# Kernel tuning notes

Hardware: AMD Instinct MI355X
Metric: run time of the kernel (lower is better)

The kernel has to match this reference:

```python
import jax, jax.numpy as jnp
import numpy as np

N = 250_000   # nodes per graph batch
E = 4_000_000 # edges
G = 1024      # graphs (segments)
F_IN, C, D = 6, 64, 5
EPS = 1e-5    # PyG LayerNorm eps


def setup_inputs() -> dict:
    key = jax.random.key(0)
    ks = jax.random.split(key, 30)
    rn = lambda k, s: jax.random.normal(k, s, jnp.float32)
    p = lambda k, s: rn(k, s) * 0.05
    return {
        "x1": rn(ks[0], (N, F_IN)),
        "edge_index1": jax.random.randint(ks[1], (2, E), 0, N, jnp.int32),
        "batch1": jnp.sort(jax.random.randint(ks[2], (N,), 0, G, jnp.int32)),
        "x2": rn(ks[3], (N, F_IN)),
        "edge_index2": jax.random.randint(ks[4], (2, E), 0, N, jnp.int32),
        "batch2": jnp.sort(jax.random.randint(ks[5], (N,), 0, G, jnp.int32)),
        "d1": rn(ks[6], (G, D)),
        "d2": rn(ks[7], (G, D)),
        # GIN MLP 1: Linear(6,64) -> ReLU -> Linear(64,64)
        "W1": p(ks[8], (F_IN, C)), "b1": jnp.zeros((C,), jnp.float32),
        "W2": p(ks[9], (C, C)),    "b2": jnp.zeros((C,), jnp.float32),
        "ln1w": jnp.ones((C,), jnp.float32), "ln1b": jnp.zeros((C,), jnp.float32),
        # GIN MLP 2
        "W3": p(ks[10], (C, C)), "b3": jnp.zeros((C,), jnp.float32),
        "W4": p(ks[11], (C, C)), "b4": jnp.zeros((C,), jnp.float32),
        "ln2w": jnp.ones((C,), jnp.float32), "ln2b": jnp.zeros((C,), jnp.float32),
        # head: Linear(138,128) -> Linear(128,64) -> Linear(64,1)
        "Wf1": p(ks[12], (2 * C + 2 * D, 128)), "bf1": jnp.zeros((128,), jnp.float32),
        "Wf2": p(ks[13], (128, 64)),            "bf2": jnp.zeros((64,), jnp.float32),
        "Wo": p(ks[14], (64, 1)),               "bo": jnp.zeros((1,), jnp.float32),
    }


def _gin(x, src, dst, Wa, ba, Wb, bb):
    # GINConv, eps=0: h = x + sum_{j in N(i)} x_j ; then MLP (dropout = eval identity)
    agg = jax.ops.segment_sum(x[src], dst, num_segments=N)
    h = x + agg
    h = jax.nn.relu(h @ Wa + ba)
    return h @ Wb + bb


def _graph_layernorm(x, batch, w, b):
    # PyG LayerNorm mode='graph': normalize over all nodes AND channels per graph
    cnt = jax.ops.segment_sum(jnp.ones((x.shape[0],), x.dtype), batch, num_segments=G)
    norm = jnp.maximum(cnt, 1.0) * x.shape[-1]          # [G]
    mean = jax.ops.segment_sum(x.sum(-1), batch, num_segments=G) / norm
    xc = x - mean[batch][:, None]
    var = jax.ops.segment_sum((xc * xc).sum(-1), batch, num_segments=G) / norm
    out = xc * jax.lax.rsqrt(var + EPS)[batch][:, None]
    return out * w + b


def _forward_one(x, edge_index, batch, W1, b1, W2, b2, ln1w, ln1b, W3, b3, W4, b4, ln2w, ln2b):
    src, dst = edge_index[0], edge_index[1]
    x = jax.nn.relu(_graph_layernorm(_gin(x, src, dst, W1, b1, W2, b2), batch, ln1w, ln1b))
    x = jax.nn.relu(_graph_layernorm(_gin(x, src, dst, W3, b3, W4, b4), batch, ln2w, ln2b))
    add = jax.ops.segment_sum(x, batch, num_segments=G)  # [G, C]
    cnt = jax.ops.segment_sum(jnp.ones((x.shape[0],), x.dtype), batch, num_segments=G)
    mean = add / jnp.maximum(cnt, 1.0)[:, None]
    return add + mean


def reference(x1, edge_index1, batch1, x2, edge_index2, batch2, d1, d2,
              W1, b1, W2, b2, ln1w, ln1b, W3, b3, W4, b4, ln2w, ln2b,
              Wf1, bf1, Wf2, bf2, Wo, bo):
    shared = (W1, b1, W2, b2, ln1w, ln1b, W3, b3, W4, b4, ln2w, ln2b)
    emb1 = _forward_one(x1, edge_index1, batch1, *shared)
    emb2 = _forward_one(x2, edge_index2, batch2, *shared)
    h = jnp.concatenate([emb1, emb2, d1, d2], axis=1)    # [G, 138]
    h = jax.nn.relu(h @ Wf1 + bf1)                       # dropout identity (eval)
    h = jax.nn.relu(h @ Wf2 + bf2)
    return h @ Wo + bo                                   # [G, 1]
```

## Files before the change

kernel.cpp:

```cpp
#include <hip/hip_runtime.h>

typedef unsigned short ushort_t;
typedef __attribute__((ext_vector_type(8))) short bf16x8;
typedef __attribute__((ext_vector_type(4))) float f32x4;

#define FIN 6
#define CAP 20480
#define LNCAP 384

__device__ __forceinline__ float blo(unsigned u) { return __uint_as_float(u << 16); }
__device__ __forceinline__ float bhi(unsigned u) { return __uint_as_float(u & 0xffff0000u); }
__device__ __forceinline__ ushort_t f2b(float f) {
  unsigned u = __float_as_uint(f);
  unsigned r = (u + 0x7fffu + ((u >> 16) & 1u)) >> 16;
  return (ushort_t)r;
}
__device__ __forceinline__ unsigned pk2(float lo, float hi) {
  return ((unsigned)f2b(hi) << 16) | (unsigned)f2b(lo);
}
union U4F { uint4 u; bf16x8 v; };
__device__ __forceinline__ bf16x8 asfrag(uint4 u) { U4F x; x.u = u; return x.v; }

__device__ __forceinline__ int xcd_swz(int b, int B) {
  int xcd = b & 7, sub = b >> 3;
  int bpx = B >> 3;
  return (xcd >> 2) * (B >> 1) + (xcd & 3) * bpx + sub;
}

#define EPT 16
#define TILE 8192

__global__ __launch_bounds__(256) void k_wpack(const float* __restrict__ W2,
    const float* __restrict__ W3, const float* __restrict__ W4, uint4* __restrict__ wfrag,
    int* __restrict__ ecur, int* __restrict__ off, int nbuk, int N2, int Etot,
    const float* __restrict__ x1, const float* __restrict__ x2,
    const int* __restrict__ batch1, const int* __restrict__ batch2,
    unsigned* __restrict__ xb, int* __restrict__ gstart, int N, int G) {
  if (blockIdx.x >= 7) {
    int G2 = 2 * G;
    int tt = (blockIdx.x - 7) * 256 + threadIdx.x;
    if (tt < N2 * 4) {
      int i = tt >> 2, k = tt & 3;
      unsigned v = 0;
      if (k < 3) {
        const float* xp = (i < N) ? (x1 + (size_t)i * 6) : (x2 + (size_t)(i - N) * 6);
        float2 f = *(const float2*)(xp + k * 2);
        v = pk2(f.x, f.y);
      }
      xb[tt] = v;
    }
    if (tt < N2) {
      int i = tt;
      int b = (i < N) ? batch1[i] : (batch2[i - N] + G);
      if (i == 0) { for (int g = 0; g <= b; ++g) gstart[g] = 0; }
      else {
        int pb = (i - 1 < N) ? batch1[i - 1] : (batch2[i - 1 - N] + G);
        for (int g = pb + 1; g <= b; ++g) gstart[g] = i;
      }
      if (i == N2 - 1) { for (int g = b + 1; g <= G2; ++g) gstart[g] = N2; }
    }
    return;
  }
  if (blockIdx.x == 6) {
    int t = threadIdx.x;
    if (t < nbuk) ecur[t] = t * CAP;
    if (t + 256 < nbuk) ecur[t + 256] = (t + 256) * CAP;
    if (t == 0) off[N2] = Etot;
    return;
  }
  int idx = blockIdx.x * 256 + threadIdx.x;
  if (idx >= 3 * 512) return;
  int widx = idx >> 9, rem = idx & 511;
  int mt = rem >> 7, kh = (rem >> 6) & 1, l = rem & 63;
  int g = l >> 4, c = l & 15;
  const float* W = (widx == 0) ? W2 : (widx == 1) ? W3 : W4;
  int k0 = kh * 32 + g * 8;
  int col = mt * 16 + c;
  uint4 v;
  v.x = pk2(W[(k0 + 0) * 64 + col], W[(k0 + 1) * 64 + col]);
  v.y = pk2(W[(k0 + 2) * 64 + col], W[(k0 + 3) * 64 + col]);
  v.z = pk2(W[(k0 + 4) * 64 + col], W[(k0 + 5) * 64 + col]);
  v.w = pk2(W[(k0 + 6) * 64 + col], W[(k0 + 7) * 64 + col]);
  wfrag[idx] = v;
}

__global__ __launch_bounds__(512) void k_bscatter(
    const int* __restrict__ src1, const int* __restrict__ dst1, int E1,
    const int* __restrict__ src2, const int* __restrict__ dst2, int E2,
    int* __restrict__ ecur, unsigned* __restrict__ ebuf, int N, int nbuk) {
  __shared__ int cnt[512];
  __shared__ int gbase[512];
  int t = threadIdx.x;
  cnt[t] = 0;
  __syncthreads();
  int tile = blockIdx.x;
  int T1 = (E1 + TILE - 1) / TILE;
  const int* srcp; const int* dstp; int Elim, ofs, base;
  if (tile < T1) { srcp = src1; dstp = dst1; Elim = E1; ofs = 0; base = tile * TILE; }
  else { srcp = src2; dstp = dst2; Elim = E2; ofs = N; base = (tile - T1) * TILE; }
  unsigned pk[EPT];
  unsigned pv[EPT];
  #pragma unroll
  for (int k = 0; k < EPT; ++k) {
    int e = base + k * 512 + t;
    if (e < Elim) {
      int d = dstp[e] + ofs;
      int b = d >> 10;
      int r = atomicAdd(&cnt[b], 1);
      pk[k] = (unsigned)b | ((unsigned)r << 9);
      pv[k] = ((unsigned)(d & 1023) << 19) | (unsigned)(srcp[e] + ofs);
    } else {
      pk[k] = 0xFFFFFFFFu;
    }
  }
  __syncthreads();
  if (t < nbuk && cnt[t] > 0) gbase[t] = atomicAdd(&ecur[t], cnt[t]);
  __syncthreads();
  #pragma unroll
  for (int k = 0; k < EPT; ++k) {
    if (pk[k] != 0xFFFFFFFFu) {
      int b = pk[k] & 511;
      int r = pk[k] >> 9;
      ebuf[gbase[b] + r] = pv[k];
    }
  }
}

__global__ __launch_bounds__(512) void k_bscan2(const int* __restrict__ ecur,
    int* __restrict__ ebase, int nbuk) {
  __shared__ int lds[512];
  int t = threadIdx.x;
  int s = (t < nbuk) ? (ecur[t] - t * CAP) : 0;
  lds[t] = s; __syncthreads();
  int acc = s;
  for (int o = 1; o < 512; o <<= 1) {
    int add = (t >= o) ? lds[t - o] : 0;
    __syncthreads();
    acc += add; lds[t] = acc;
    __syncthreads();
  }
  if (t < nbuk) ebase[t] = acc - s;
}

__global__ __launch_bounds__(256) void k_bcsr(const unsigned* __restrict__ ebuf,
    const int* __restrict__ ecur, const int* __restrict__ ebase,
    int* __restrict__ off, int* __restrict__ csr, int N2) {
  __shared__ int hist[1024];
  __shared__ int lofs[1024];
  __shared__ int sc[256];
  int b = blockIdx.x, t = threadIdx.x;
  int nb0 = b << 10;
  int bn = N2 - nb0; if (bn > 1024) bn = 1024;
  int s_beg = b * CAP, s_end = ecur[b];
  int base = ebase[b];
  #pragma unroll
  for (int k = 0; k < 4; ++k) hist[t * 4 + k] = 0;
  __syncthreads();
  for (int e = s_beg + t; e < s_end; e += 256) atomicAdd(&hist[ebuf[e] >> 19], 1);
  __syncthreads();
  int h0 = hist[t * 4 + 0], h1 = hist[t * 4 + 1], h2 = hist[t * 4 + 2], h3 = hist[t * 4 + 3];
  int s = h0 + h1 + h2 + h3;
  sc[t] = s; __syncthreads();
  int acc = s;
  for (int o = 1; o < 256; o <<= 1) {
    int add = (t >= o) ? sc[t - o] : 0;
    __syncthreads();
    acc += add; sc[t] = acc;
    __syncthreads();
  }
  int run = acc - s;
  lofs[t * 4 + 0] = run; run += h0;
  lofs[t * 4 + 1] = run; run += h1;
  lofs[t * 4 + 2] = run; run += h2;
  lofs[t * 4 + 3] = run;
  __syncthreads();
  #pragma unroll
  for (int k = 0; k < 4; ++k) {
    int j = t * 4 + k;
    if (j < bn) off[nb0 + j] = base + lofs[j];
  }
  __syncthreads();
  for (int e = s_beg + t; e < s_end; e += 256) {
    unsigned p = ebuf[e];
    int r = atomicAdd(&lofs[p >> 19], 1);
    csr[base + r] = (int)(p & 0x7FFFFu);
  }
}

#define ACC6(u) { a0 += blo(u.x); a1 += bhi(u.x); a2 += blo(u.y); a3 += bhi(u.y); a4 += blo(u.z); a5 += bhi(u.z); }
__global__ __launch_bounds__(256) void k_gin1f(const uint4* __restrict__ xb4,
    const int* __restrict__ off, const int* __restrict__ csr,
    const float* __restrict__ W1, const float* __restrict__ b1,
    const uint4* __restrict__ wf2, const float* __restrict__ b2,
    ushort_t* __restrict__ hr, int n) {
  __shared__ __align__(16) ushort_t t1s[32][72];
  __shared__ float sh[4][8][FIN];
  int t = threadIdx.x, w = t >> 6, lane = t & 63;
  int nd = lane >> 3, sl = lane & 7;
  int blk = xcd_swz(blockIdx.x, gridDim.x);
  int nb0 = blk * 32;
  int i = nb0 + w * 8 + nd;

  float w1r[FIN];
  #pragma unroll
  for (int k = 0; k < FIN; ++k) w1r[k] = W1[k * 64 + lane];
  float bb1 = b1[lane];

  float a0 = 0, a1 = 0, a2 = 0, a3 = 0, a4 = 0, a5 = 0;
  if (i < n) {
    int e0 = off[i], e1 = off[i + 1];
    int e = e0 + sl;
    for (; e + 8 < e1; e += 16) {
      uint4 u = xb4[csr[e]];
      uint4 v = xb4[csr[e + 8]];
      ACC6(u); ACC6(v);
    }
    if (e < e1) { uint4 u = xb4[csr[e]]; ACC6(u); }
    if (sl == 0) { uint4 u = xb4[i]; ACC6(u); }
  }
  #pragma unroll
  for (int m = 1; m < 8; m <<= 1) {
    a0 += __shfl_xor(a0, m); a1 += __shfl_xor(a1, m); a2 += __shfl_xor(a2, m);
    a3 += __shfl_xor(a3, m); a4 += __shfl_xor(a4, m); a5 += __shfl_xor(a5, m);
  }
  if (sl < FIN) {
    float v = (sl == 0) ? a0 : (sl == 1) ? a1 : (sl == 2) ? a2 : (sl == 3) ? a3 : (sl == 4) ? a4 : a5;
    sh[w][nd][sl] = v;
  }
  #pragma unroll
  for (int nd2 = 0; nd2 < 8; ++nd2) {
    float h = bb1;
    #pragma unroll
    for (int k = 0; k < FIN; ++k) h = fmaf(sh[w][nd2][k], w1r[k], h);
    t1s[w * 8 + nd2][lane] = f2b(fmaxf(h, 0.f));
  }
  __syncthreads();
  if (w < 2) {
    int g = lane >> 4, c = lane & 15;
    bf16x8 af[4][2];
    #pragma unroll
    for (int mt = 0; mt < 4; ++mt)
      #pragma unroll
      for (int kh = 0; kh < 2; ++kh) af[mt][kh] = asfrag(wf2[(mt * 2 + kh) * 64 + lane]);
    int r0 = w * 16 + c;
    bf16x8 bf0 = asfrag(*(const uint4*)&t1s[r0][8 * g]);
    bf16x8 bf1 = asfrag(*(const uint4*)&t1s[r0][8 * g + 32]);
    f32x4 acc[4];
    #pragma unroll
    for (int mt = 0; mt < 4; ++mt) {
      acc[mt] = (f32x4){b2[mt * 16 + 4 * g + 0], b2[mt * 16 + 4 * g + 1],
                        b2[mt * 16 + 4 * g + 2], b2[mt * 16 + 4 * g + 3]};
      acc[mt] = __builtin_amdgcn_mfma_f32_16x16x32_bf16(af[mt][0], bf0, acc[mt], 0, 0, 0);
      acc[mt] = __builtin_amdgcn_mfma_f32_16x16x32_bf16(af[mt][1], bf1, acc[mt], 0, 0, 0);
    }
    #pragma unroll
    for (int mt = 0; mt < 4; ++mt) {
      uint2 pv;
      pv.x = pk2(acc[mt][0], acc[mt][1]);
      pv.y = pk2(acc[mt][2], acc[mt][3]);
      *(uint2*)&t1s[r0][mt * 16 + 4 * g] = pv;
    }
    int n2 = lane >> 2, ch = (lane & 3) * 16;
    uint4 s0 = *(const uint4*)&t1s[w * 16 + n2][ch];
    uint4 s1 = *(const uint4*)&t1s[w * 16 + n2][ch + 8];
    int orow = nb0 + w * 16 + n2;
    if (orow < n) {
      uint4* op = (uint4*)(hr + (size_t)orow * 64);
      op[(lane & 3) * 2] = s0;
      op[(lane & 3) * 2 + 1] = s1;
    }
  }
}

__device__ __forceinline__ float2 up2(unsigned v) { return make_float2(blo(v), bhi(v)); }
#define PACC(u) { float2 q0 = up2(u.x), q1 = up2(u.y), q2 = up2(u.z), q3 = up2(u.w); \
                  c0.x += q0.x; c0.y += q0.y; c1.x += q1.x; c1.y += q1.y; \
                  c2.x += q2.x; c2.y += q2.y; c3.x += q3.x; c3.y += q3.y; }
__global__ __launch_bounds__(256) void k_agg64(const ushort_t* __restrict__ hb,
    const int* __restrict__ off, const int* __restrict__ csr,
    ushort_t* __restrict__ aggb, int n) {
  int t = threadIdx.x, w = t >> 6, lane = t & 63;
  int blk = xcd_swz(blockIdx.x, gridDim.x);
  int i = blk * 4 + w;
  if (i >= n) return;
  int grp = lane >> 3, sl = lane & 7;
  int e0 = off[i], e1 = off[i + 1];
  const uint4* hb4 = (const uint4*)hb;
  float2 c0 = {0, 0}, c1 = {0, 0}, c2 = {0, 0}, c3 = {0, 0};
  int e = e0 + grp;
  for (; e + 8 < e1; e += 16) {
    int sa = csr[e], sb = csr[e + 8];
    uint4 ua = hb4[(size_t)sa * 8 + sl];
    uint4 ub = hb4[(size_t)sb * 8 + sl];
    PACC(ua); PACC(ub);
  }
  if (e < e1) {
    int sa = csr[e];
    uint4 ua = hb4[(size_t)sa * 8 + sl];
    PACC(ua);
  }
  #pragma unroll
  for (int m = 8; m < 64; m <<= 1) {
    c0.x += __shfl_xor(c0.x, m); c0.y += __shfl_xor(c0.y, m);
    c1.x += __shfl_xor(c1.x, m); c1.y += __shfl_xor(c1.y, m);
    c2.x += __shfl_xor(c2.x, m); c2.y += __shfl_xor(c2.y, m);
    c3.x += __shfl_xor(c3.x, m); c3.y += __shfl_xor(c3.y, m);
  }
  if (grp == 0) {
    uint4 us = hb4[(size_t)i * 8 + sl];
    PACC(us);
    uint4 o;
    o.x = pk2(c0.x, c0.y); o.y = pk2(c1.x, c1.y);
    o.z = pk2(c2.x, c2.y); o.w = pk2(c3.x, c3.y);
    ((uint4*)aggb)[(size_t)i * 8 + sl] = o;
  }
}

__global__ __launch_bounds__(256) void k_mlp2_mfma(const ushort_t* __restrict__ aggb,
    const uint4* __restrict__ wf3, const float* __restrict__ b3,
    const uint4* __restrict__ wf4, const float* __restrict__ b4,
    ushort_t* __restrict__ zb, int n) {
  __shared__ __align__(16) ushort_t lds[4][16][72];
  int t = threadIdx.x, w = t >> 6, l = t & 63;
  int g = l >> 4, c = l & 15;
  bf16x8 a3[4][2], a4[4][2];
  #pragma unroll
  for (int mt = 0; mt < 4; ++mt)
    #pragma unroll
    for (int kh = 0; kh < 2; ++kh) {
      a3[mt][kh] = asfrag(wf3[(mt * 2 + kh) * 64 + l]);
      a4[mt][kh] = asfrag(wf4[(mt * 2 + kh) * 64 + l]);
    }
  float bs3[4][4], bs4[4][4];
  #pragma unroll
  for (int mt = 0; mt < 4; ++mt)
    #pragma unroll
    for (int r = 0; r < 4; ++r) {
      bs3[mt][r] = b3[mt * 16 + 4 * g + r];
      bs4[mt][r] = b4[mt * 16 + 4 * g + r];
    }
  int ntile = (n + 15) >> 4;
  for (int tau = blockIdx.x * 4 + w; tau < ntile; tau += gridDim.x * 4) {
    int nb = tau << 4;
    int row = nb + c; if (row >= n) row = n - 1;
    const uint4* rp = (const uint4*)(aggb + (size_t)row * 64);
    bf16x8 bf0 = asfrag(rp[g]);
    bf16x8 bf1 = asfrag(rp[g + 4]);
    f32x4 acc[4];
    #pragma unroll
    for (int mt = 0; mt < 4; ++mt) {
      acc[mt] = (f32x4){bs3[mt][0], bs3[mt][1], bs3[mt][2], bs3[mt][3]};
      acc[mt] = __builtin_amdgcn_mfma_f32_16x16x32_bf16(a3[mt][0], bf0, acc[mt], 0, 0, 0);
      acc[mt] = __builtin_amdgcn_mfma_f32_16x16x32_bf16(a3[mt][1], bf1, acc[mt], 0, 0, 0);
    }
    #pragma unroll
    for (int mt = 0; mt < 4; ++mt) {
      uint2 pv;
      pv.x = pk2(fmaxf(acc[mt][0], 0.f), fmaxf(acc[mt][1], 0.f));
      pv.y = pk2(fmaxf(acc[mt][2], 0.f), fmaxf(acc[mt][3], 0.f));
      *(uint2*)&lds[w][c][mt * 16 + 4 * g] = pv;
    }
    bf16x8 h0 = asfrag(*(const uint4*)&lds[w][c][8 * g]);
    bf16x8 h1 = asfrag(*(const uint4*)&lds[w][c][8 * g + 32]);
    f32x4 ac2[4];
    #pragma unroll
    for (int mt = 0; mt < 4; ++mt) {
      ac2[mt] = (f32x4){bs4[mt][0], bs4[mt][1], bs4[mt][2], bs4[mt][3]};
      ac2[mt] = __builtin_amdgcn_mfma_f32_16x16x32_bf16(a4[mt][0], h0, ac2[mt], 0, 0, 0);
      ac2[mt] = __builtin_amdgcn_mfma_f32_16x16x32_bf16(a4[mt][1], h1, ac2[mt], 0, 0, 0);
    }
    #pragma unroll
    for (int mt = 0; mt < 4; ++mt) {
      uint2 pv;
      pv.x = pk2(ac2[mt][0], ac2[mt][1]);
      pv.y = pk2(ac2[mt][2], ac2[mt][3]);
      *(uint2*)&lds[w][c][mt * 16 + 4 * g] = pv;
    }
    int n2 = l >> 2, ch = (l & 3) * 16;
    uint4 s0 = *(const uint4*)&lds[w][n2][ch];
    uint4 s1 = *(const uint4*)&lds[w][n2][ch + 8];
    int orow = nb + n2;
    if (orow < n) {
      uint4* op = (uint4*)(zb + (size_t)orow * 64);
      op[(l & 3) * 2] = s0;
      op[(l & 3) * 2 + 1] = s1;
    }
  }
}

__global__ __launch_bounds__(256) void k_ln1(ushort_t* __restrict__ hr,
    const int* __restrict__ gstart, const float* __restrict__ w, const float* __restrict__ bb) {
  __shared__ uint4 st[LNCAP * 8];
  __shared__ float l1[256], l2[256];
  __shared__ float mm[2];
  int g = blockIdx.x, t = threadIdx.x;
  int s0 = gstart[g], s1 = gstart[g + 1], cnt = s1 - s0;
  uint4* src = (uint4*)hr + (size_t)s0 * 8;
  int nch = cnt * 8;
  bool fit = cnt <= LNCAP;
  float s = 0.f, ss = 0.f;
  for (int j = t; j < nch; j += 256) {
    uint4 u = src[j];
    if (fit) st[j] = u;
    float v0 = blo(u.x), v1 = bhi(u.x), v2 = blo(u.y), v3 = bhi(u.y);
    float v4 = blo(u.z), v5 = bhi(u.z), v6 = blo(u.w), v7 = bhi(u.w);
    s += ((v0 + v1) + (v2 + v3)) + ((v4 + v5) + (v6 + v7));
    ss += ((v0 * v0 + v1 * v1) + (v2 * v2 + v3 * v3)) + ((v4 * v4 + v5 * v5) + (v6 * v6 + v7 * v7));
  }
  l1[t] = s; l2[t] = ss;
  __syncthreads();
  for (int o = 128; o > 0; o >>= 1) {
    if (t < o) { l1[t] += l1[t + o]; l2[t] += l2[t + o]; }
    __syncthreads();
  }
  if (t == 0) {
    float cf = (float)cnt;
    float norm = fmaxf(cf, 1.f) * 64.f;
    float mean = l1[0] / norm;
    float var = fmaxf(l2[0] / norm - mean * mean, 0.f);
    mm[0] = mean; mm[1] = rsqrtf(var + 1e-5f);
  }
  __syncthreads();
  float mean = mm[0], inv = mm[1];
  for (int j = t; j < nch; j += 256) {
    uint4 u = fit ? st[j] : src[j];
    int q = j & 7;
    float4 w0 = *(const float4*)(w + q * 8);
    float4 w1 = *(const float4*)(w + q * 8 + 4);
    float4 c0 = *(const float4*)(bb + q * 8);
    float4 c1 = *(const float4*)(bb + q * 8 + 4);
    uint4 o;
    o.x = pk2(fmaxf((blo(u.x) - mean) * inv * w0.x + c0.x, 0.f),
              fmaxf((bhi(u.x) - mean) * inv * w0.y + c0.y, 0.f));
    o.y = pk2(fmaxf((blo(u.y) - mean) * inv * w0.z + c0.z, 0.f),
              fmaxf((bhi(u.y) - mean) * inv * w0.w + c0.w, 0.f));
    o.z = pk2(fmaxf((blo(u.z) - mean) * inv * w1.x + c1.x, 0.f),
              fmaxf((bhi(u.z) - mean) * inv * w1.y + c1.y, 0.f));
    o.w = pk2(fmaxf((blo(u.w) - mean) * inv * w1.z + c1.z, 0.f),
              fmaxf((bhi(u.w) - mean) * inv * w1.w + c1.w, 0.f));
    src[j] = o;
  }
}

__global__ __launch_bounds__(256) void k_ln2pool(const ushort_t* __restrict__ zb,
    const int* __restrict__ gstart, const float* __restrict__ w, const float* __restrict__ bb,
    float* __restrict__ emb) {
  __shared__ unsigned st[LNCAP * 32];
  __shared__ float l1[256], l2[256];
  __shared__ float mm[2];
  int g = blockIdx.x, t = threadIdx.x;
  int s0 = gstart[g], s1 = gstart[g + 1], cnt = s1 - s0;
  const unsigned* src = (const unsigned*)zb + (size_t)s0 * 32;
  int nu = cnt * 32;
  bool fit = cnt <= LNCAP;
  float s = 0.f, ss = 0.f;
  for (int j = t; j < nu; j += 256) {
    unsigned u = src[j];
    if (fit) st[j] = u;
    float v0 = blo(u), v1 = bhi(u);
    s += v0 + v1;
    ss += v0 * v0 + v1 * v1;
  }
  l1[t] = s; l2[t] = ss;
  __syncthreads();
  for (int o = 128; o > 0; o >>= 1) {
    if (t < o) { l1[t] += l1[t + o]; l2[t] += l2[t + o]; }
    __syncthreads();
  }
  if (t == 0) {
    float cf = (float)cnt;
    float norm = fmaxf(cf, 1.f) * 64.f;
    float mean = l1[0] / norm;
    float var = fmaxf(l2[0] / norm - mean * mean, 0.f);
    mm[0] = mean; mm[1] = rsqrtf(var + 1e-5f);
  }
  __syncthreads();
  float mean = mm[0], inv = mm[1];
  int c2 = t & 31, sub = t >> 5;
  float w0 = w[c2 * 2], w1 = w[c2 * 2 + 1], b0 = bb[c2 * 2], b1v = bb[c2 * 2 + 1];
  float acc0 = 0.f, acc1 = 0.f;
  for (int i = sub; i < cnt; i += 8) {
    unsigned u = fit ? st[i * 32 + c2] : src[(size_t)i * 32 + c2];
    acc0 += fmaxf((blo(u) - mean) * inv * w0 + b0, 0.f);
    acc1 += fmaxf((bhi(u) - mean) * inv * w1 + b1v, 0.f);
  }
  __syncthreads();
  l1[t] = acc0; l2[t] = acc1;
  __syncthreads();
  if (sub == 0) {
    float t0 = 0.f, t1v = 0.f;
    #pragma unroll
    for (int sx = 0; sx < 8; ++sx) { t0 += l1[sx * 32 + c2]; t1v += l2[sx * 32 + c2]; }
    float cf = fmaxf((float)cnt, 1.f);
    emb[g * 64 + c2 * 2]     = t0 + t0 / cf;
    emb[g * 64 + c2 * 2 + 1] = t1v + t1v / cf;
  }
}

__global__ __launch_bounds__(128) void k_head(const float* __restrict__ emb1,
    const float* __restrict__ emb2, const float* __restrict__ d1, const float* __restrict__ d2,
    const float* __restrict__ Wf1, const float* __restrict__ bf1,
    const float* __restrict__ Wf2, const float* __restrict__ bf2,
    const float* __restrict__ Wo, const float* __restrict__ bo, float* __restrict__ out) {
  int g = blockIdx.x, t = threadIdx.x;
  __shared__ float v[138], h1s[128], h2s[64];
  if (t < 64) v[t] = emb1[g * 64 + t];
  else v[t] = emb2[g * 64 + (t - 64)];
  if (t < 5) v[128 + t] = d1[g * 5 + t];
  else if (t < 10) v[133 + (t - 5)] = d2[g * 5 + (t - 5)];
  __syncthreads();
  float a = bf1[t];
  for (int k = 0; k < 138; ++k) a = fmaf(v[k], Wf1[k * 128 + t], a);
  h1s[t] = fmaxf(a, 0.f);
  __syncthreads();
  if (t < 64) {
    float a2 = bf2[t];
    #pragma unroll 8
    for (int k = 0; k < 128; ++k) a2 = fmaf(h1s[k], Wf2[k * 64 + t], a2);
    h2s[t] = fmaxf(a2, 0.f);
  }
  __syncthreads();
  if (t == 0) {
    float s = bo[0];
    for (int k = 0; k < 64; ++k) s += h2s[k] * Wo[k];
    out[g] = s;
  }
}

extern "C" void kernel_launch(void* const* d_in, const int* in_sizes, int n_in,
                              void* d_out, int out_size, void* d_ws, size_t ws_size,
                              hipStream_t stream) {
  const float* x1     = (const float*)d_in[0];
  const int*   ei1    = (const int*)d_in[1];
  const int*   batch1 = (const int*)d_in[2];
  const float* x2     = (const float*)d_in[3];
  const int*   ei2    = (const int*)d_in[4];
  const int*   batch2 = (const int*)d_in[5];
  const float* d1     = (const float*)d_in[6];
  const float* d2     = (const float*)d_in[7];
  const float* W1  = (const float*)d_in[8],  *b1  = (const float*)d_in[9];
  const float* W2  = (const float*)d_in[10], *b2  = (const float*)d_in[11];
  const float* ln1w = (const float*)d_in[12], *ln1b = (const float*)d_in[13];
  const float* W3  = (const float*)d_in[14], *b3  = (const float*)d_in[15];
  const float* W4  = (const float*)d_in[16], *b4  = (const float*)d_in[17];
  const float* ln2w = (const float*)d_in[18], *ln2b = (const float*)d_in[19];
  const float* Wf1 = (const float*)d_in[20], *bf1 = (const float*)d_in[21];
  const float* Wf2 = (const float*)d_in[22], *bf2 = (const float*)d_in[23];
  const float* Wo  = (const float*)d_in[24], *bo  = (const float*)d_in[25];
  float* out = (float*)d_out;

  const int N = in_sizes[0] / FIN;
  const int G = in_sizes[6] / 5;
  const int E1 = in_sizes[1] / 2;
  const int E2 = in_sizes[4] / 2;
  const int N2 = 2 * N;
  const int Etot = E1 + E2;
  const int NBUK = (N2 + 1023) >> 10;

  char* p = (char*)d_ws;
  auto alloc = [&](size_t bytes) { void* r = p; p += (bytes + 255) & ~(size_t)255; return r; };
  int*      off    = (int*)alloc((size_t)(N2 + 1) * 4);
  int*      ecur   = (int*)alloc(512 * 4);
  int*      ebase  = (int*)alloc(513 * 4);
  int*      csr    = (int*)alloc((size_t)Etot * 4);
  int*      gstart = (int*)alloc((size_t)(2 * G + 1) * 4);
  uint4*    wfrag  = (uint4*)alloc(3 * 512 * 16);
  ushort_t* bufA   = (ushort_t*)alloc((size_t)N2 * 64 * 2);
  ushort_t* bufB   = (ushort_t*)alloc((size_t)N2 * 64 * 2);
  float*    emb    = (float*)alloc((size_t)2 * G * 64 * 4);

  unsigned* xb   = (unsigned*)bufB;
  unsigned* ebuf = (unsigned*)((char*)bufB + (size_t)N2 * 16);
  ushort_t* hr   = bufA;
  ushort_t* aggb = bufB;
  ushort_t* zb   = bufA;

  const uint4* wf2 = wfrag;
  const uint4* wf3 = wfrag + 512;
  const uint4* wf4 = wfrag + 1024;

  const int SCAT   = (E1 + TILE - 1) / TILE + (E2 + TILE - 1) / TILE;
  const int GRID_F = (((N2 + 31) / 32) + 7) & ~7;
  const int GRID_W = (((N2 + 3) / 4) + 7) & ~7;
  const int GRID_P = (N2 * 4 + 255) / 256;

  k_wpack<<<7 + GRID_P, 256, 0, stream>>>(W2, W3, W4, wfrag, ecur, off, NBUK, N2, Etot,
                                          x1, x2, batch1, batch2, xb, gstart, N, G);
  k_bscatter<<<SCAT, 512, 0, stream>>>(ei1, ei1 + E1, E1, ei2, ei2 + E2, E2, ecur, ebuf, N, NBUK);
  k_bscan2<<<1, 512, 0, stream>>>(ecur, ebase, NBUK);
  k_bcsr<<<NBUK, 256, 0, stream>>>(ebuf, ecur, ebase, off, csr, N2);

  k_gin1f<<<GRID_F, 256, 0, stream>>>((const uint4*)xb, off, csr, W1, b1, wf2, b2, hr, N2);
  k_ln1<<<2 * G, 256, 0, stream>>>(hr, gstart, ln1w, ln1b);
  k_agg64<<<GRID_W, 256, 0, stream>>>(hr, off, csr, aggb, N2);
  k_mlp2_mfma<<<2048, 256, 0, stream>>>(aggb, wf3, b3, wf4, b4, zb, N2);
  k_ln2pool<<<2 * G, 256, 0, stream>>>(zb, gstart, ln2w, ln2b, emb);

  k_head<<<G, 128, 0, stream>>>(emb, emb + (size_t)G * 64, d1, d2, Wf1, bf1, Wf2, bf2, Wo, bo, out);
}
```

Measured before the change: 547.7 us.

## Split destination buckets into source-range sub-buckets to sort CSR by source

```diff
diff --git a/kernel.cpp b/kernel.cpp
--- a/kernel.cpp
+++ b/kernel.cpp
@@ -5,7 +5,8 @@
 typedef __attribute__((ext_vector_type(4))) float f32x4;
 
 #define FIN 6
-#define CAP 20480
+#define CAPS 1408
+#define NSUBMAX 8192
 #define LNCAP 384
 
 __device__ __forceinline__ float blo(unsigned u) { return __uint_as_float(u << 16); }
@@ -32,7 +33,7 @@
 
 __global__ __launch_bounds__(256) void k_wpack(const float* __restrict__ W2,
     const float* __restrict__ W3, const float* __restrict__ W4, uint4* __restrict__ wfrag,
-    int* __restrict__ ecur, int* __restrict__ off, int nbuk, int N2, int Etot,
+    int* __restrict__ ecur, int* __restrict__ off, int N2, int Etot,
     const float* __restrict__ x1, const float* __restrict__ x2,
     const int* __restrict__ batch1, const int* __restrict__ batch2,
     unsigned* __restrict__ xb, int* __restrict__ gstart, int N, int G) {
@@ -62,10 +63,8 @@
     return;
   }
   if (blockIdx.x == 6) {
-    int t = threadIdx.x;
-    if (t < nbuk) ecur[t] = t * CAP;
-    if (t + 256 < nbuk) ecur[t + 256] = (t + 256) * CAP;
-    if (t == 0) off[N2] = Etot;
+    for (int j = threadIdx.x; j < NSUBMAX; j += 256) ecur[j] = j * CAPS;
+    if (threadIdx.x == 0) off[N2] = Etot;
     return;
   }
   int idx = blockIdx.x * 256 + threadIdx.x;
@@ -87,11 +86,10 @@
 __global__ __launch_bounds__(512) void k_bscatter(
     const int* __restrict__ src1, const int* __restrict__ dst1, int E1,
     const int* __restrict__ src2, const int* __restrict__ dst2, int E2,
-    int* __restrict__ ecur, unsigned* __restrict__ ebuf, int N, int nbuk) {
-  __shared__ int cnt[512];
-  __shared__ int gbase[512];
+    int* __restrict__ ecur, unsigned* __restrict__ ebuf, int N, int nsub) {
+  __shared__ int cnt[NSUBMAX];
   int t = threadIdx.x;
-  cnt[t] = 0;
+  for (int j = t; j < NSUBMAX; j += 512) cnt[j] = 0;
   __syncthreads();
   int tile = blockIdx.x;
   int T1 = (E1 + TILE - 1) / TILE;
@@ -104,24 +102,28 @@
   for (int k = 0; k < EPT; ++k) {
     int e = base + k * 512 + t;
     if (e < Elim) {
+      int sl = srcp[e];
       int d = dstp[e] + ofs;
-      int b = d >> 10;
-      int r = atomicAdd(&cnt[b], 1);
-      pk[k] = (unsigned)b | ((unsigned)r << 9);
-      pv[k] = ((unsigned)(d & 1023) << 19) | (unsigned)(srcp[e] + ofs);
+      int sub = ((d >> 10) << 4) | (sl >> 14);
+      int r = atomicAdd(&cnt[sub], 1);
+      pk[k] = (unsigned)sub | ((unsigned)r << 13);
+      pv[k] = ((unsigned)(d & 1023) << 19) | (unsigned)(sl + ofs);
     } else {
       pk[k] = 0xFFFFFFFFu;
     }
   }
   __syncthreads();
-  if (t < nbuk && cnt[t] > 0) gbase[t] = atomicAdd(&ecur[t], cnt[t]);
+  for (int j = t; j < nsub; j += 512) {
+    int c = cnt[j];
+    if (c > 0) cnt[j] = atomicAdd(&ecur[j], c);
+  }
   __syncthreads();
   #pragma unroll
   for (int k = 0; k < EPT; ++k) {
     if (pk[k] != 0xFFFFFFFFu) {
-      int b = pk[k] & 511;
-      int r = pk[k] >> 9;
-      ebuf[gbase[b] + r] = pv[k];
+      int sub = pk[k] & (NSUBMAX - 1);
+      int r = pk[k] >> 13;
+      ebuf[cnt[sub] + r] = pv[k];
     }
   }
 }
@@ -130,7 +132,14 @@
     int* __restrict__ ebase, int nbuk) {
   __shared__ int lds[512];
   int t = threadIdx.x;
-  int s = (t < nbuk) ? (ecur[t] - t * CAP) : 0;
+  int s = 0;
+  if (t < nbuk) {
+    #pragma unroll
+    for (int sl = 0; sl < 16; ++sl) {
+      int sub = t * 16 + sl;
+      s += ecur[sub] - sub * CAPS;
+    }
+  }
   lds[t] = s; __syncthreads();
   int acc = s;
   for (int o = 1; o < 512; o <<= 1) {
@@ -151,12 +160,15 @@
   int b = blockIdx.x, t = threadIdx.x;
   int nb0 = b << 10;
   int bn = N2 - nb0; if (bn > 1024) bn = 1024;
-  int s_beg = b * CAP, s_end = ecur[b];
   int base = ebase[b];
   #pragma unroll
   for (int k = 0; k < 4; ++k) hist[t * 4 + k] = 0;
   __syncthreads();
-  for (int e = s_beg + t; e < s_end; e += 256) atomicAdd(&hist[ebuf[e] >> 19], 1);
+  for (int sl = 0; sl < 16; ++sl) {
+    int sub = (b << 4) | sl;
+    int s_beg = sub * CAPS, s_end = ecur[sub];
+    for (int e = s_beg + t; e < s_end; e += 256) atomicAdd(&hist[ebuf[e] >> 19], 1);
+  }
   __syncthreads();
   int h0 = hist[t * 4 + 0], h1 = hist[t * 4 + 1], h2 = hist[t * 4 + 2], h3 = hist[t * 4 + 3];
   int s = h0 + h1 + h2 + h3;
@@ -180,10 +192,15 @@
     if (j < bn) off[nb0 + j] = base + lofs[j];
   }
   __syncthreads();
-  for (int e = s_beg + t; e < s_end; e += 256) {
-    unsigned p = ebuf[e];
-    int r = atomicAdd(&lofs[p >> 19], 1);
-    csr[base + r] = (int)(p & 0x7FFFFu);
+  for (int sl = 0; sl < 16; ++sl) {
+    int sub = (b << 4) | sl;
+    int s_beg = sub * CAPS, s_end = ecur[sub];
+    for (int e = s_beg + t; e < s_end; e += 256) {
+      unsigned p = ebuf[e];
+      int r = atomicAdd(&lofs[p >> 19], 1);
+      csr[base + r] = (int)(p & 0x7FFFFu);
+    }
+    __syncthreads();
   }
 }
 
@@ -556,11 +573,12 @@
   const int N2 = 2 * N;
   const int Etot = E1 + E2;
   const int NBUK = (N2 + 1023) >> 10;
+  const int NSUB = NBUK * 16;
 
   char* p = (char*)d_ws;
   auto alloc = [&](size_t bytes) { void* r = p; p += (bytes + 255) & ~(size_t)255; return r; };
   int*      off    = (int*)alloc((size_t)(N2 + 1) * 4);
-  int*      ecur   = (int*)alloc(512 * 4);
+  int*      ecur   = (int*)alloc((size_t)NSUBMAX * 4);
   int*      ebase  = (int*)alloc(513 * 4);
   int*      csr    = (int*)alloc((size_t)Etot * 4);
   int*      gstart = (int*)alloc((size_t)(2 * G + 1) * 4);
@@ -584,9 +602,9 @@
   const int GRID_W = (((N2 + 3) / 4) + 7) & ~7;
   const int GRID_P = (N2 * 4 + 255) / 256;
 
-  k_wpack<<<7 + GRID_P, 256, 0, stream>>>(W2, W3, W4, wfrag, ecur, off, NBUK, N2, Etot,
+  k_wpack<<<7 + GRID_P, 256, 0, stream>>>(W2, W3, W4, wfrag, ecur, off, N2, Etot,
                                           x1, x2, batch1, batch2, xb, gstart, N, G);
-  k_bscatter<<<SCAT, 512, 0, stream>>>(ei1, ei1 + E1, E1, ei2, ei2 + E2, E2, ecur, ebuf, N, NBUK);
+  k_bscatter<<<SCAT, 512, 0, stream>>>(ei1, ei1 + E1, E1, ei2, ei2 + E2, E2, ecur, ebuf, N, NSUB);
   k_bscan2<<<1, 512, 0, stream>>>(ecur, ebase, NBUK);
   k_bcsr<<<NBUK, 256, 0, stream>>>(ebuf, ecur, ebase, off, csr, N2);
 
```

After: 607.4 us. +10.9%, slower.
